# Performance work log

Measured on AMD Instinct MI355X. Metric: run time of the kernel, lower is better.

The kernel has to match this reference:

```python
import jax, jax.numpy as jnp
import numpy as np

B, S, E, H = 2, 2048, 1024, 16
HD = E // H  # head_dim = 64


def setup_inputs() -> dict:
    key = jax.random.key(0)
    k1, k2, k3, k4, k5 = jax.random.split(key, 5)
    return {
        "hidden_states": jax.random.normal(k1, (B, S, E), dtype=jnp.float32),
        "w_attn": jax.random.normal(k2, (E, 3 * E), dtype=jnp.float32) * 0.02,
        "b_attn": jax.random.normal(k3, (3 * E,), dtype=jnp.float32) * 0.02,
        "w_proj": jax.random.normal(k4, (E, E), dtype=jnp.float32) * 0.02,
        "b_proj": jax.random.normal(k5, (E,), dtype=jnp.float32) * 0.02,
    }


def reference(hidden_states, w_attn, b_attn, w_proj, b_proj):
    b, s, e = hidden_states.shape
    # QKV projection (HF Conv1D: x @ W + b)
    qkv = hidden_states @ w_attn + b_attn  # [B,S,3E]
    q, k, v = jnp.split(qkv, 3, axis=-1)
    # [B,S,E] -> [B,H,S,HD]
    def split_heads(x):
        return x.reshape(b, s, H, HD).transpose(0, 2, 1, 3)
    q, k, v = split_heads(q), split_heads(k), split_heads(v)
    scale = 1.0 / float(HD) ** 0.5  # scale_attn_weights
    scores = jnp.einsum("bhqd,bhkd->bhqk", q, k) * scale  # [B,H,S,S]
    causal = jnp.tril(jnp.ones((s, s), dtype=bool))
    mask_value = jnp.finfo(scores.dtype).min
    scores = jnp.where(causal, scores, mask_value)
    attn = jax.nn.softmax(scores, axis=-1)
    # attn_dropout is identity (p=0.0)
    out = jnp.einsum("bhqk,bhkd->bhqd", attn, v)  # [B,H,S,HD]
    out = out.transpose(0, 2, 1, 3).reshape(b, s, e)  # merge heads
    out = out @ w_proj + b_proj  # c_proj; resid_dropout identity
    return out
```

## Files before the change

### kernel.cpp

```cpp
#include <hip/hip_runtime.h>
#include <hip/hip_bf16.h>

#define B_   2
#define S_   2048
#define E_   1024
#define H_   16
#define HD_  64
#define E3_  3072
#define M_   4096
#define QKS  2048
#define QSC  0.1803368801111f

using short8 = __attribute__((ext_vector_type(8))) short;
using f32x4  = __attribute__((ext_vector_type(4))) float;

__device__ __forceinline__ unsigned short f2bf(float f) {
  union { float f; unsigned v; } t; t.f = f;
  unsigned r = t.v + 0x7FFFu + ((t.v >> 16) & 1u);
  return (unsigned short)(r >> 16);
}

__device__ __forceinline__ float exp2_fast(float x) {
  float r;
  asm("v_exp_f32 %0, %1" : "=v"(r) : "v"(x));
  return r;
}

__device__ __forceinline__ void gload16(const void* g, void* l) {
  __builtin_amdgcn_global_load_lds(
      (const __attribute__((address_space(1))) unsigned int*)g,
      (__attribute__((address_space(3))) unsigned int*)l, 16, 0, 0);
}

__global__ __launch_bounds__(256) void prep(
    const float* __restrict__ X, const float* __restrict__ Wa,
    const float* __restrict__ Wp,
    unsigned short* __restrict__ Xb, unsigned short* __restrict__ WaT,
    unsigned short* __restrict__ WpT) {
  __shared__ float tile[32][33];
  const int id = blockIdx.x;
  if (id < 4096) {
    const int i = (id * 256 + threadIdx.x) * 4;
    float4 v = *(const float4*)(X + i);
    ushort4 o;
    o.x = f2bf(v.x); o.y = f2bf(v.y); o.z = f2bf(v.z); o.w = f2bf(v.w);
    *(ushort4*)(Xb + i) = o;
  } else {
    const float* W; unsigned short* WT; int N, bn, bk;
    if (id < 7168) {
      W = Wa; WT = WaT; N = E3_;
      const int j = id - 4096; bn = (j % 96) * 32; bk = (j / 96) * 32;
    } else {
      W = Wp; WT = WpT; N = E_;
      const int j = id - 7168; bn = (j & 31) * 32; bk = (j >> 5) * 32;
    }
    const int tx = threadIdx.x & 31, ty = threadIdx.x >> 5;
    #pragma unroll
    for (int i2 = 0; i2 < 32; i2 += 8)
      tile[ty + i2][tx] = W[(size_t)(bk + ty + i2) * N + bn + tx];
    __syncthreads();
    #pragma unroll
    for (int i2 = 0; i2 < 32; i2 += 8)
      WT[(size_t)(bn + ty + i2) * E_ + bk + tx] = f2bf(tile[tx][ty + i2]);
  }
}

template <int MODE>
__global__ __launch_bounds__(256) void gemm_bt_bias(
    const unsigned short* __restrict__ A,
    const unsigned short* __restrict__ BT,
    const float* __restrict__ bias,
    float* __restrict__ Cf,
    unsigned short* __restrict__ Cbf,
    unsigned short* __restrict__ Vt,
    int M, int N, int K) {
  __shared__ __align__(16) unsigned short As[128 * 64];
  __shared__ __align__(16) unsigned short Bs[128 * 64];
  const int t = threadIdx.x;
  const int lane = t & 63, w = t >> 6;
  const int wr = w >> 1, wc = w & 1;
  const int m0 = blockIdx.y * 128, n0 = blockIdx.x * 128;
  const int lrow = lane & 15, lkg = lane >> 4;
  const int srow = t >> 3;
  const int sc8  = (t & 7) * 8;
  const int sgc  = sc8 ^ (((t >> 3) & 7) << 3);

  f32x4 acc[4][4];
  const f32x4 z = {0.f, 0.f, 0.f, 0.f};
  #pragma unroll
  for (int i = 0; i < 4; ++i)
    #pragma unroll
    for (int j = 0; j < 4; ++j) acc[i][j] = z;

  for (int k0 = 0; k0 < K; k0 += 64) {
    __syncthreads();
    #pragma unroll
    for (int p = 0; p < 4; ++p) {
      const int r = srow + 32 * p;
      gload16(A  + (size_t)(m0 + r) * K + k0 + sgc, &As[r * 64 + sc8]);
      gload16(BT + (size_t)(n0 + r) * K + k0 + sgc, &Bs[r * 64 + sc8]);
    }
    __syncthreads();

    short8 af[4][2], bf[4][2];
    #pragma unroll
    for (int m = 0; m < 4; ++m) {
      const int row = wr * 64 + m * 16 + lrow;
      const int base = row * 64, sw = (row & 7) << 3;
      af[m][0] = *(const short8*)&As[base + ((lkg * 8) ^ sw)];
      af[m][1] = *(const short8*)&As[base + ((32 + lkg * 8) ^ sw)];
    }
    #pragma unroll
    for (int n = 0; n < 4; ++n) {
      const int row = wc * 64 + n * 16 + lrow;
      const int base = row * 64, sw = (row & 7) << 3;
      bf[n][0] = *(const short8*)&Bs[base + ((lkg * 8) ^ sw)];
      bf[n][1] = *(const short8*)&Bs[base + ((32 + lkg * 8) ^ sw)];
    }
    #pragma unroll
    for (int m = 0; m < 4; ++m)
      #pragma unroll
      for (int n = 0; n < 4; ++n) {
        acc[m][n] = __builtin_amdgcn_mfma_f32_16x16x32_bf16(af[m][0], bf[n][0],
                                                            acc[m][n], 0, 0, 0);
        acc[m][n] = __builtin_amdgcn_mfma_f32_16x16x32_bf16(af[m][1], bf[n][1],
                                                            acc[m][n], 0, 0, 0);
      }
  }

  const int r0 = (lane >> 4) * 4, c0 = lane & 15;
  #pragma unroll
  for (int m = 0; m < 4; ++m) {
    #pragma unroll
    for (int n = 0; n < 4; ++n) {
      const int row = m0 + wr * 64 + m * 16 + r0;
      const int col = n0 + wc * 64 + n * 16 + c0;
      const float bv = bias[col];
      if (MODE == 0) {
        #pragma unroll
        for (int r = 0; r < 4; ++r)
          Cf[(size_t)(row + r) * N + col] = acc[m][n][r] + bv;
      } else {
        if (col < 2 * E_) {
          const float sc = (col < E_) ? QSC : 1.0f;
          #pragma unroll
          for (int r = 0; r < 4; ++r)
            Cbf[(size_t)(row + r) * QKS + col] = f2bf((acc[m][n][r] + bv) * sc);
        } else {
          const int hd = col - 2 * E_;
          ushort4 o;
          o.x = f2bf(acc[m][n][0] + bv);
          o.y = f2bf(acc[m][n][1] + bv);
          o.z = f2bf(acc[m][n][2] + bv);
          o.w = f2bf(acc[m][n][3] + bv);
          *(ushort4*)&Vt[(((size_t)(row >> 11) * H_ + (hd >> 6)) * HD_ +
                          (hd & 63)) * (size_t)S_ + (row & 2047)] = o;
        }
      }
    }
  }
}

__global__ __launch_bounds__(256) void flash_attn(
    const unsigned short* __restrict__ qk,
    const unsigned short* __restrict__ Vt,
    unsigned short* __restrict__ aout,
    float* __restrict__ Opart,
    float* __restrict__ Lpart) {
  __shared__ __align__(16) unsigned short Ks[2][64 * 64];
  __shared__ __align__(16) unsigned short Vs[2][64 * 64];

  const int t = threadIdx.x, lane = t & 63, w = t >> 6;
  const int bh = blockIdx.x;
  const int yy = blockIdx.y;
  int qt, lo, hi, part = 0;
  bool split = false;
  if (yy < 8) {
    qt = 23 - yy; lo = 0; hi = qt + 1;
  } else if (yy < 24) {
    const int idx = yy - 8;
    qt = 31 - (idx >> 1); part = idx & 1;
    const int mid = (qt + 2) >> 1;
    lo = part ? mid : 0; hi = part ? qt + 1 : mid;
    split = true;
  } else {
    qt = 39 - yy; lo = 0; hi = qt + 1;
  }
  const int b = bh >> 4, h = bh & 15;
  const int lq = lane & 15;
  const int g  = lane >> 4;
  const int lk8 = g * 8;
  const int swzq = (lq & 7) << 3;
  const size_t basebs = (size_t)b * S_;
  const f32x4 z = {0.f, 0.f, 0.f, 0.f};

  short8 qf[2];
  {
    const int qrow = qt * 64 + w * 16 + lq;
    const unsigned short* qp = qk + (basebs + qrow) * QKS + h * HD_;
    qf[0] = *(const short8*)(qp + lk8);
    qf[1] = *(const short8*)(qp + 32 + lk8);
  }

  float l_q = 0.f;
  f32x4 o_acc[4];
  #pragma unroll
  for (int n = 0; n < 4; ++n) o_acc[n] = z;

  const int sr = t >> 3, scc = (t & 7) * 8;
  const unsigned short* kp0 =
      qk + (basebs + sr) * QKS + E_ + h * HD_ + (scc ^ ((sr & 7) << 3));
  const unsigned short* kp1 = kp0 + 32 * QKS;
  const unsigned short* vp0 =
      Vt + ((size_t)bh * HD_ + sr) * S_ + (scc ^ ((sr & 7) << 3));
  const unsigned short* vp1 = vp0 + 32 * S_;

  auto stage = [&](int buf, int kt) {
    const size_t koff = (size_t)kt * 64 * QKS;
    const size_t voff = (size_t)kt * 64;
    gload16(kp0 + koff, &Ks[buf][t * 8]);
    gload16(kp1 + koff, &Ks[buf][t * 8 + 2048]);
    gload16(vp0 + voff, &Vs[buf][t * 8]);
    gload16(vp1 + voff, &Vs[buf][t * 8 + 2048]);
  };

  stage(0, lo);
  __syncthreads();
  int cur = 0;

  for (int kt = lo; kt < hi; ++kt) {
    if (kt + 1 < hi) stage(cur ^ 1, kt + 1);

    f32x4 st[4];
    __builtin_amdgcn_s_setprio(1);
    #pragma unroll
    for (int f = 0; f < 4; ++f) {
      const int rowb = (f * 16 + lq) * 64;
      short8 kf0 = *(const short8*)&Ks[cur][rowb + (lk8 ^ swzq)];
      short8 kf1 = *(const short8*)&Ks[cur][rowb + ((lk8 + 32) ^ swzq)];
      st[f] = __builtin_amdgcn_mfma_f32_16x16x32_bf16(kf0, qf[0], z, 0, 0, 0);
      st[f] = __builtin_amdgcn_mfma_f32_16x16x32_bf16(kf1, qf[1], st[f], 0, 0, 0);
    }
    __builtin_amdgcn_s_setprio(0);

    if (kt == qt) {
      const int qcol = w * 16 + lq;
      #pragma unroll
      for (int f = 0; f < 4; ++f)
        #pragma unroll
        for (int r = 0; r < 4; ++r)
          if (16 * f + 4 * g + r > qcol) st[f][r] = -1e30f;
    }

    unsigned pw[4][2];
    #pragma unroll
    for (int f = 0; f < 4; ++f) {
      float p0 = exp2_fast(st[f][0]);
      float p1 = exp2_fast(st[f][1]);
      float p2 = exp2_fast(st[f][2]);
      float p3 = exp2_fast(st[f][3]);
      l_q += (p0 + p1) + (p2 + p3);
      asm("v_cvt_pk_bf16_f32 %0, %1, %2" : "=v"(pw[f][0]) : "v"(p0), "v"(p1));
      asm("v_cvt_pk_bf16_f32 %0, %1, %2" : "=v"(pw[f][1]) : "v"(p2), "v"(p3));
    }

    unsigned c1a = pw[0][0], c1b = pw[1][0];
    unsigned c2a = pw[0][1], c2b = pw[1][1];
    unsigned c3a = pw[2][0], c3b = pw[3][0];
    unsigned c4a = pw[2][1], c4b = pw[3][1];
    asm("v_permlane32_swap_b32 %0, %1" : "+v"(c1a), "+v"(c1b));
    asm("v_permlane16_swap_b32 %0, %1" : "+v"(c1a), "+v"(c1b));
    asm("v_permlane32_swap_b32 %0, %1" : "+v"(c2a), "+v"(c2b));
    asm("v_permlane16_swap_b32 %0, %1" : "+v"(c2a), "+v"(c2b));
    asm("v_permlane32_swap_b32 %0, %1" : "+v"(c3a), "+v"(c3b));
    asm("v_permlane16_swap_b32 %0, %1" : "+v"(c3a), "+v"(c3b));
    asm("v_permlane32_swap_b32 %0, %1" : "+v"(c4a), "+v"(c4b));
    asm("v_permlane16_swap_b32 %0, %1" : "+v"(c4a), "+v"(c4b));
    union U8 { unsigned u[4]; short8 s; };
    U8 pa0u = {{c1a, c2a, c1b, c2b}};
    U8 pa1u = {{c3a, c4a, c3b, c4b}};
    const short8 pa0 = pa0u.s, pa1 = pa1u.s;

    __builtin_amdgcn_s_setprio(1);
    #pragma unroll
    for (int n = 0; n < 4; ++n) {
      const int rowb = (n * 16 + lq) * 64;
      short8 vb0 = *(const short8*)&Vs[cur][rowb + (lk8 ^ swzq)];
      short8 vb1 = *(const short8*)&Vs[cur][rowb + ((lk8 + 32) ^ swzq)];
      o_acc[n] = __builtin_amdgcn_mfma_f32_16x16x32_bf16(pa0, vb0, o_acc[n], 0, 0, 0);
      o_acc[n] = __builtin_amdgcn_mfma_f32_16x16x32_bf16(pa1, vb1, o_acc[n], 0, 0, 0);
    }
    __builtin_amdgcn_s_setprio(0);

    __syncthreads();
    cur ^= 1;
  }

  l_q += __shfl_xor(l_q, 16);
  l_q += __shfl_xor(l_q, 32);

  if (!split) {
    const int qbase = qt * 64 + w * 16 + 4 * g;
    #pragma unroll
    for (int r = 0; r < 4; ++r) {
      const float lr = __shfl(l_q, 4 * g + r);
      const float inv = 1.0f / lr;
      const int row = qbase + r;
      #pragma unroll
      for (int n = 0; n < 4; ++n)
        aout[(basebs + row) * E_ + h * HD_ + n * 16 + lq] =
            f2bf(o_acc[n][r] * inv);
    }
  } else {
    const int sidx = (bh << 3) | (qt - 24);
    float* Ob = Opart + ((size_t)(sidx * 2 + part) << 12);
    #pragma unroll
    for (int r = 0; r < 4; ++r) {
      const int qrow = w * 16 + 4 * g + r;
      #pragma unroll
      for (int n = 0; n < 4; ++n)
        Ob[qrow * 64 + n * 16 + lq] = o_acc[n][r];
    }
    if (g == 0)
      Lpart[(sidx * 2 + part) * 64 + w * 16 + lq] = l_q;
  }
}

__global__ __launch_bounds__(256) void attn_combine(
    const float* __restrict__ Opart, const float* __restrict__ Lpart,
    unsigned short* __restrict__ aout) {
  const int s = blockIdx.x;
  const int bh = s >> 3, qt = 24 + (s & 7);
  const int b = bh >> 4, h = bh & 15;
  const int t = threadIdx.x;
  const int q = t >> 2;
  const int d0 = (t & 3) * 16;
  const float l = Lpart[(s * 2 + 0) * 64 + q] + Lpart[(s * 2 + 1) * 64 + q];
  const float inv = 1.0f / l;
  const float* p0 = Opart + ((size_t)(s * 2 + 0) << 12) + q * 64 + d0;
  const float* p1 = Opart + ((size_t)(s * 2 + 1) << 12) + q * 64 + d0;
  unsigned short* dst =
      aout + ((size_t)b * S_ + qt * 64 + q) * E_ + h * HD_ + d0;
  #pragma unroll
  for (int i = 0; i < 16; ++i)
    dst[i] = f2bf((p0[i] + p1[i]) * inv);
}

extern "C" void kernel_launch(void* const* d_in, const int* in_sizes, int n_in,
                              void* d_out, int out_size, void* d_ws, size_t ws_size,
                              hipStream_t stream) {
  const float* X  = (const float*)d_in[0];
  const float* Wa = (const float*)d_in[1];
  const float* ba = (const float*)d_in[2];
  const float* Wp = (const float*)d_in[3];
  const float* bp = (const float*)d_in[4];
  float* out = (float*)d_out;

  char* ws = (char*)d_ws;
  unsigned short* Xb  = (unsigned short*)ws; ws += (size_t)M_ * E_ * 2;
  unsigned short* WaT = (unsigned short*)ws; ws += (size_t)E3_ * E_ * 2;
  unsigned short* WpT = (unsigned short*)ws; ws += (size_t)E_ * E_ * 2;
  unsigned short* QK  = (unsigned short*)ws; ws += (size_t)M_ * QKS * 2;
  unsigned short* Vt  = (unsigned short*)ws; ws += (size_t)M_ * E_ * 2;
  unsigned short* AO  = (unsigned short*)ws; ws += (size_t)M_ * E_ * 2;
  float* Opart = (float*)ws; ws += (size_t)256 * 2 * 64 * 64 * 4;
  float* Lpart = (float*)ws; ws += (size_t)256 * 2 * 64 * 4;

  prep<<<8192, 256, 0, stream>>>(X, Wa, Wp, Xb, WaT, WpT);
  gemm_bt_bias<1><<<dim3(E3_ / 128, M_ / 128), 256, 0, stream>>>(
      Xb, WaT, ba, nullptr, QK, Vt, M_, E3_, E_);
  flash_attn<<<dim3(B_ * H_, 40), 256, 0, stream>>>(QK, Vt, AO, Opart, Lpart);
  attn_combine<<<256, 256, 0, stream>>>(Opart, Lpart, AO);
  gemm_bt_bias<0><<<dim3(E_ / 128, M_ / 128), 256, 0, stream>>>(
      AO, WpT, bp, out, nullptr, nullptr, M_, E_, E_);
}
```

Before: 104.4 us.

## Use 128-row query tiles with 8 waves per block in flash attention

Flash attention moves from 64-query tiles with 4 waves to 128-query tiles with 8 waves, so each staged 64-key K/V tile is shared by twice as many query rows. Each thread now issues one async load per K and V tile instead of two. Upper-half waves skip the fully masked diagonal tile, and the split/combine scheme is rebalanced over 24 y-blocks. Partial outputs are stored in bf16 rather than fp32 to cut combine traffic, at a small cost in precision. The grid shrinks, which may reduce occupancy and load balance across CUs.

```diff
diff --git a/kernel.cpp b/kernel.cpp
--- a/kernel.cpp
+++ b/kernel.cpp
@@ -18,6 +18,10 @@
   union { float f; unsigned v; } t; t.f = f;
   unsigned r = t.v + 0x7FFFu + ((t.v >> 16) & 1u);
   return (unsigned short)(r >> 16);
+}
+
+__device__ __forceinline__ float bf2f(unsigned short u) {
+  union { unsigned v; float f; } t; t.v = ((unsigned)u) << 16; return t.f;
 }
 
 __device__ __forceinline__ float exp2_fast(float x) {
@@ -161,11 +165,11 @@
   }
 }
 
-__global__ __launch_bounds__(256) void flash_attn(
+__global__ __launch_bounds__(512) void flash_attn(
     const unsigned short* __restrict__ qk,
     const unsigned short* __restrict__ Vt,
     unsigned short* __restrict__ aout,
-    float* __restrict__ Opart,
+    unsigned short* __restrict__ Opart,
     float* __restrict__ Lpart) {
   __shared__ __align__(16) unsigned short Ks[2][64 * 64];
   __shared__ __align__(16) unsigned short Vs[2][64 * 64];
@@ -176,15 +180,13 @@
   int qt, lo, hi, part = 0;
   bool split = false;
   if (yy < 8) {
-    qt = 23 - yy; lo = 0; hi = qt + 1;
-  } else if (yy < 24) {
-    const int idx = yy - 8;
-    qt = 31 - (idx >> 1); part = idx & 1;
-    const int mid = (qt + 2) >> 1;
-    lo = part ? mid : 0; hi = part ? qt + 1 : mid;
-    split = true;
+    qt = yy; lo = 0; hi = 2 * qt + 2;
+  } else if (yy < 16) {
+    qt = 15 - (yy - 8); part = 0; split = true;
+    lo = 0; hi = qt + 1;
   } else {
-    qt = 39 - yy; lo = 0; hi = qt + 1;
+    qt = 15 - (yy - 16); part = 1; split = true;
+    lo = qt + 1; hi = 2 * qt + 2;
   }
   const int b = bh >> 4, h = bh & 15;
   const int lq = lane & 15;
@@ -196,7 +198,7 @@
 
   short8 qf[2];
   {
-    const int qrow = qt * 64 + w * 16 + lq;
+    const int qrow = qt * 128 + w * 16 + lq;
     const unsigned short* qp = qk + (basebs + qrow) * QKS + h * HD_;
     qf[0] = *(const short8*)(qp + lk8);
     qf[1] = *(const short8*)(qp + 32 + lk8);
@@ -207,21 +209,16 @@
   #pragma unroll
   for (int n = 0; n < 4; ++n) o_acc[n] = z;
 
-  const int sr = t >> 3, scc = (t & 7) * 8;
-  const unsigned short* kp0 =
+  const int sr = t >> 3;
+  const int scc = (t & 7) * 8;
+  const unsigned short* kp =
       qk + (basebs + sr) * QKS + E_ + h * HD_ + (scc ^ ((sr & 7) << 3));
-  const unsigned short* kp1 = kp0 + 32 * QKS;
-  const unsigned short* vp0 =
+  const unsigned short* vp =
       Vt + ((size_t)bh * HD_ + sr) * S_ + (scc ^ ((sr & 7) << 3));
-  const unsigned short* vp1 = vp0 + 32 * S_;
 
   auto stage = [&](int buf, int kt) {
-    const size_t koff = (size_t)kt * 64 * QKS;
-    const size_t voff = (size_t)kt * 64;
-    gload16(kp0 + koff, &Ks[buf][t * 8]);
-    gload16(kp1 + koff, &Ks[buf][t * 8 + 2048]);
-    gload16(vp0 + voff, &Vs[buf][t * 8]);
-    gload16(vp1 + voff, &Vs[buf][t * 8 + 2048]);
+    gload16(kp + (size_t)kt * 64 * QKS, &Ks[buf][t * 8]);
+    gload16(vp + (size_t)kt * 64,       &Vs[buf][t * 8]);
   };
 
   stage(0, lo);
@@ -231,66 +228,71 @@
   for (int kt = lo; kt < hi; ++kt) {
     if (kt + 1 < hi) stage(cur ^ 1, kt + 1);
 
-    f32x4 st[4];
-    __builtin_amdgcn_s_setprio(1);
-    #pragma unroll
-    for (int f = 0; f < 4; ++f) {
-      const int rowb = (f * 16 + lq) * 64;
-      short8 kf0 = *(const short8*)&Ks[cur][rowb + (lk8 ^ swzq)];
-      short8 kf1 = *(const short8*)&Ks[cur][rowb + ((lk8 + 32) ^ swzq)];
-      st[f] = __builtin_amdgcn_mfma_f32_16x16x32_bf16(kf0, qf[0], z, 0, 0, 0);
-      st[f] = __builtin_amdgcn_mfma_f32_16x16x32_bf16(kf1, qf[1], st[f], 0, 0, 0);
-    }
-    __builtin_amdgcn_s_setprio(0);
-
-    if (kt == qt) {
-      const int qcol = w * 16 + lq;
-      #pragma unroll
-      for (int f = 0; f < 4; ++f)
+    const int krel = kt - 2 * qt;
+    const bool skip = (krel == 1) && (w < 4);
+    if (!skip) {
+      f32x4 st[4];
+      __builtin_amdgcn_s_setprio(1);
+      #pragma unroll
+      for (int f = 0; f < 4; ++f) {
+        const int rowb = (f * 16 + lq) * 64;
+        short8 kf0 = *(const short8*)&Ks[cur][rowb + (lk8 ^ swzq)];
+        short8 kf1 = *(const short8*)&Ks[cur][rowb + ((lk8 + 32) ^ swzq)];
+        st[f] = __builtin_amdgcn_mfma_f32_16x16x32_bf16(kf0, qf[0], z, 0, 0, 0);
+        st[f] = __builtin_amdgcn_mfma_f32_16x16x32_bf16(kf1, qf[1], st[f], 0, 0, 0);
+      }
+      __builtin_amdgcn_s_setprio(0);
+
+      if (krel >= 0) {
+        const int qcol = w * 16 + lq;
+        const int kbase = krel * 64;
         #pragma unroll
-        for (int r = 0; r < 4; ++r)
-          if (16 * f + 4 * g + r > qcol) st[f][r] = -1e30f;
-    }
-
-    unsigned pw[4][2];
-    #pragma unroll
-    for (int f = 0; f < 4; ++f) {
-      float p0 = exp2_fast(st[f][0]);
-      float p1 = exp2_fast(st[f][1]);
-      float p2 = exp2_fast(st[f][2]);
-      float p3 = exp2_fast(st[f][3]);
-      l_q += (p0 + p1) + (p2 + p3);
-      asm("v_cvt_pk_bf16_f32 %0, %1, %2" : "=v"(pw[f][0]) : "v"(p0), "v"(p1));
-      asm("v_cvt_pk_bf16_f32 %0, %1, %2" : "=v"(pw[f][1]) : "v"(p2), "v"(p3));
-    }
-
-    unsigned c1a = pw[0][0], c1b = pw[1][0];
-    unsigned c2a = pw[0][1], c2b = pw[1][1];
-    unsigned c3a = pw[2][0], c3b = pw[3][0];
-    unsigned c4a = pw[2][1], c4b = pw[3][1];
-    asm("v_permlane32_swap_b32 %0, %1" : "+v"(c1a), "+v"(c1b));
-    asm("v_permlane16_swap_b32 %0, %1" : "+v"(c1a), "+v"(c1b));
-    asm("v_permlane32_swap_b32 %0, %1" : "+v"(c2a), "+v"(c2b));
-    asm("v_permlane16_swap_b32 %0, %1" : "+v"(c2a), "+v"(c2b));
-    asm("v_permlane32_swap_b32 %0, %1" : "+v"(c3a), "+v"(c3b));
-    asm("v_permlane16_swap_b32 %0, %1" : "+v"(c3a), "+v"(c3b));
-    asm("v_permlane32_swap_b32 %0, %1" : "+v"(c4a), "+v"(c4b));
-    asm("v_permlane16_swap_b32 %0, %1" : "+v"(c4a), "+v"(c4b));
-    union U8 { unsigned u[4]; short8 s; };
-    U8 pa0u = {{c1a, c2a, c1b, c2b}};
-    U8 pa1u = {{c3a, c4a, c3b, c4b}};
-    const short8 pa0 = pa0u.s, pa1 = pa1u.s;
-
-    __builtin_amdgcn_s_setprio(1);
-    #pragma unroll
-    for (int n = 0; n < 4; ++n) {
-      const int rowb = (n * 16 + lq) * 64;
-      short8 vb0 = *(const short8*)&Vs[cur][rowb + (lk8 ^ swzq)];
-      short8 vb1 = *(const short8*)&Vs[cur][rowb + ((lk8 + 32) ^ swzq)];
-      o_acc[n] = __builtin_amdgcn_mfma_f32_16x16x32_bf16(pa0, vb0, o_acc[n], 0, 0, 0);
-      o_acc[n] = __builtin_amdgcn_mfma_f32_16x16x32_bf16(pa1, vb1, o_acc[n], 0, 0, 0);
-    }
-    __builtin_amdgcn_s_setprio(0);
+        for (int f = 0; f < 4; ++f)
+          #pragma unroll
+          for (int r = 0; r < 4; ++r)
+            if (kbase + 16 * f + 4 * g + r > qcol) st[f][r] = -1e30f;
+      }
+
+      unsigned pw[4][2];
+      #pragma unroll
+      for (int f = 0; f < 4; ++f) {
+        float p0 = exp2_fast(st[f][0]);
+        float p1 = exp2_fast(st[f][1]);
+        float p2 = exp2_fast(st[f][2]);
+        float p3 = exp2_fast(st[f][3]);
+        l_q += (p0 + p1) + (p2 + p3);
+        asm("v_cvt_pk_bf16_f32 %0, %1, %2" : "=v"(pw[f][0]) : "v"(p0), "v"(p1));
+        asm("v_cvt_pk_bf16_f32 %0, %1, %2" : "=v"(pw[f][1]) : "v"(p2), "v"(p3));
+      }
+
+      unsigned c1a = pw[0][0], c1b = pw[1][0];
+      unsigned c2a = pw[0][1], c2b = pw[1][1];
+      unsigned c3a = pw[2][0], c3b = pw[3][0];
+      unsigned c4a = pw[2][1], c4b = pw[3][1];
+      asm("v_permlane32_swap_b32 %0, %1" : "+v"(c1a), "+v"(c1b));
+      asm("v_permlane16_swap_b32 %0, %1" : "+v"(c1a), "+v"(c1b));
+      asm("v_permlane32_swap_b32 %0, %1" : "+v"(c2a), "+v"(c2b));
+      asm("v_permlane16_swap_b32 %0, %1" : "+v"(c2a), "+v"(c2b));
+      asm("v_permlane32_swap_b32 %0, %1" : "+v"(c3a), "+v"(c3b));
+      asm("v_permlane16_swap_b32 %0, %1" : "+v"(c3a), "+v"(c3b));
+      asm("v_permlane32_swap_b32 %0, %1" : "+v"(c4a), "+v"(c4b));
+      asm("v_permlane16_swap_b32 %0, %1" : "+v"(c4a), "+v"(c4b));
+      union U8 { unsigned u[4]; short8 s; };
+      U8 pa0u = {{c1a, c2a, c1b, c2b}};
+      U8 pa1u = {{c3a, c4a, c3b, c4b}};
+      const short8 pa0 = pa0u.s, pa1 = pa1u.s;
+
+      __builtin_amdgcn_s_setprio(1);
+      #pragma unroll
+      for (int n = 0; n < 4; ++n) {
+        const int rowb = (n * 16 + lq) * 64;
+        short8 vb0 = *(const short8*)&Vs[cur][rowb + (lk8 ^ swzq)];
+        short8 vb1 = *(const short8*)&Vs[cur][rowb + ((lk8 + 32) ^ swzq)];
+        o_acc[n] = __builtin_amdgcn_mfma_f32_16x16x32_bf16(pa0, vb0, o_acc[n], 0, 0, 0);
+        o_acc[n] = __builtin_amdgcn_mfma_f32_16x16x32_bf16(pa1, vb1, o_acc[n], 0, 0, 0);
+      }
+      __builtin_amdgcn_s_setprio(0);
+    }
 
     __syncthreads();
     cur ^= 1;
@@ -300,7 +302,7 @@
   l_q += __shfl_xor(l_q, 32);
 
   if (!split) {
-    const int qbase = qt * 64 + w * 16 + 4 * g;
+    const int qbase = qt * 128 + w * 16 + 4 * g;
     #pragma unroll
     for (int r = 0; r < 4; ++r) {
       const float lr = __shfl(l_q, 4 * g + r);
@@ -312,38 +314,38 @@
             f2bf(o_acc[n][r] * inv);
     }
   } else {
-    const int sidx = (bh << 3) | (qt - 24);
-    float* Ob = Opart + ((size_t)(sidx * 2 + part) << 12);
+    const int sidx = (bh << 3) | (qt - 8);
+    unsigned short* Ob = Opart + ((size_t)(sidx * 2 + part) << 13);
     #pragma unroll
     for (int r = 0; r < 4; ++r) {
       const int qrow = w * 16 + 4 * g + r;
       #pragma unroll
       for (int n = 0; n < 4; ++n)
-        Ob[qrow * 64 + n * 16 + lq] = o_acc[n][r];
+        Ob[qrow * 64 + n * 16 + lq] = f2bf(o_acc[n][r]);
     }
     if (g == 0)
-      Lpart[(sidx * 2 + part) * 64 + w * 16 + lq] = l_q;
+      Lpart[(sidx * 2 + part) * 128 + w * 16 + lq] = l_q;
   }
 }
 
 __global__ __launch_bounds__(256) void attn_combine(
-    const float* __restrict__ Opart, const float* __restrict__ Lpart,
+    const unsigned short* __restrict__ Opart, const float* __restrict__ Lpart,
     unsigned short* __restrict__ aout) {
   const int s = blockIdx.x;
-  const int bh = s >> 3, qt = 24 + (s & 7);
+  const int bh = s >> 3, qtb = 8 + (s & 7);
   const int b = bh >> 4, h = bh & 15;
   const int t = threadIdx.x;
-  const int q = t >> 2;
-  const int d0 = (t & 3) * 16;
-  const float l = Lpart[(s * 2 + 0) * 64 + q] + Lpart[(s * 2 + 1) * 64 + q];
+  const int q = t >> 1;
+  const int d0 = (t & 1) * 32;
+  const float l = Lpart[(s * 2 + 0) * 128 + q] + Lpart[(s * 2 + 1) * 128 + q];
   const float inv = 1.0f / l;
-  const float* p0 = Opart + ((size_t)(s * 2 + 0) << 12) + q * 64 + d0;
-  const float* p1 = Opart + ((size_t)(s * 2 + 1) << 12) + q * 64 + d0;
+  const unsigned short* p0 = Opart + ((size_t)(s * 2 + 0) << 13) + q * 64 + d0;
+  const unsigned short* p1 = Opart + ((size_t)(s * 2 + 1) << 13) + q * 64 + d0;
   unsigned short* dst =
-      aout + ((size_t)b * S_ + qt * 64 + q) * E_ + h * HD_ + d0;
+      aout + ((size_t)b * S_ + qtb * 128 + q) * E_ + h * HD_ + d0;
   #pragma unroll
-  for (int i = 0; i < 16; ++i)
-    dst[i] = f2bf((p0[i] + p1[i]) * inv);
+  for (int i = 0; i < 32; ++i)
+    dst[i] = f2bf((bf2f(p0[i]) + bf2f(p1[i])) * inv);
 }
 
 extern "C" void kernel_launch(void* const* d_in, const int* in_sizes, int n_in,
@@ -363,13 +365,14 @@
   unsigned short* QK  = (unsigned short*)ws; ws += (size_t)M_ * QKS * 2;
   unsigned short* Vt  = (unsigned short*)ws; ws += (size_t)M_ * E_ * 2;
   unsigned short* AO  = (unsigned short*)ws; ws += (size_t)M_ * E_ * 2;
-  float* Opart = (float*)ws; ws += (size_t)256 * 2 * 64 * 64 * 4;
-  float* Lpart = (float*)ws; ws += (size_t)256 * 2 * 64 * 4;
+  unsigned short* Opart = (unsigned short*)ws;
+  ws += (size_t)256 * 2 * 128 * 64 * 2;
+  float* Lpart = (float*)ws; ws += (size_t)256 * 2 * 128 * 4;
 
   prep<<<8192, 256, 0, stream>>>(X, Wa, Wp, Xb, WaT, WpT);
   gemm_bt_bias<1><<<dim3(E3_ / 128, M_ / 128), 256, 0, stream>>>(
       Xb, WaT, ba, nullptr, QK, Vt, M_, E3_, E_);
-  flash_attn<<<dim3(B_ * H_, 40), 256, 0, stream>>>(QK, Vt, AO, Opart, Lpart);
+  flash_attn<<<dim3(B_ * H_, 24), 512, 0, stream>>>(QK, Vt, AO, Opart, Lpart);
   attn_combine<<<256, 256, 0, stream>>>(Opart, Lpart, AO);
   gemm_bt_bias<0><<<dim3(E_ / 128, M_ / 128), 256, 0, stream>>>(
       AO, WpT, bp, out, nullptr, nullptr, M_, E_, E_);
```

New measurement: 101.9 us. -2.4%, faster.
